# Kernel tuning notes

Hardware: AMD Instinct MI355X
Metric: run time of the kernel (lower is better)

Reference implementation:

```python
import jax, jax.numpy as jnp
import numpy as np

B, L, E, H = 2, 2048, 1024, 16
D = E // H  # head_dim = 64


def setup_inputs() -> dict:
    key = jax.random.key(0)
    ks = jax.random.split(key, 9)
    s = 1.0 / np.sqrt(E)
    return {
        "query": jax.random.normal(ks[0], (B, L, E), jnp.float32),
        "key": jax.random.normal(ks[1], (B, L, E), jnp.float32),
        "value": jax.random.normal(ks[2], (B, L, E), jnp.float32),
        # torch Linear weights are [out_features, in_features]
        "Wq": jax.random.uniform(ks[3], (E, E), jnp.float32, -s, s),
        "bq": jnp.zeros((E,), jnp.float32),
        "Wk": jax.random.uniform(ks[4], (E, E), jnp.float32, -s, s),  # k_proj, no bias (add_bias_kv=False)
        "Wv": jax.random.uniform(ks[5], (E, E), jnp.float32, -s, s),  # v_proj, no bias
        "Wo": jax.random.uniform(ks[6], (E, E), jnp.float32, -s, s),
        "bo": jnp.zeros((E,), jnp.float32),
    }


def reference(query, key, value, Wq, bq, Wk, Wv, Wo, bo):
    # Projections (torch Linear: y = x @ W.T + b)
    q = query @ Wq.T + bq          # [B, L, E]
    k = key @ Wk.T                 # [B, L, E]
    v = value @ Wv.T               # [B, L, E]
    # Split heads
    q = q.reshape(B, L, H, D)
    k = k.reshape(B, L, H, D)
    v = v.reshape(B, L, H, D)
    # Scaled dot-product attention; the source's chunked online-softmax
    # computes exactly softmax(q k^T / sqrt(D)) v.
    q = q / jnp.sqrt(jnp.asarray(D, q.dtype))
    scores = jnp.einsum("bqhd,bkhd->bhqk", q, k)      # [B, H, L, L]
    probs = jax.nn.softmax(scores, axis=-1)
    out = jnp.einsum("bhqk,bkhd->bqhd", probs, v)     # [B, L, H, D]
    out = out.reshape(B, L, E)
    return out @ Wo.T + bo
```

## Files before the change

### kernel.cpp

```cpp
#include <hip/hip_runtime.h>

typedef __bf16 bf16;
typedef __bf16 bf16x8 __attribute__((ext_vector_type(8)));
typedef __bf16 bf16x4 __attribute__((ext_vector_type(4)));
typedef float  f32x4  __attribute__((ext_vector_type(4)));

#define MFMA_BF16(a, b, c) __builtin_amdgcn_mfma_f32_16x16x32_bf16((a), (b), (c), 0, 0, 0)


__device__ __forceinline__ void async_load16(const bf16* g, const bf16* l) {
    auto gp = (const __attribute__((address_space(1))) unsigned int*)(unsigned long long)(const void*)g;
    auto lp = (__attribute__((address_space(3))) unsigned int*)(unsigned int)(unsigned long long)(const void*)l;
    __builtin_amdgcn_global_load_lds(gp, lp, 16, 0, 0);
}

__global__ void cvt_bf16_kernel(
    const float* __restrict__ s0, const float* __restrict__ s1, const float* __restrict__ s2,
    const float* __restrict__ s3, const float* __restrict__ s4, const float* __restrict__ s5,
    const float* __restrict__ s6,
    bf16* __restrict__ d0, bf16* __restrict__ d1, bf16* __restrict__ d2,
    bf16* __restrict__ d3, bf16* __restrict__ d4, bf16* __restrict__ d5,
    bf16* __restrict__ d6)
{
    unsigned e = (blockIdx.x * 256 + threadIdx.x) * 4;
    const float* src; bf16* dst; unsigned off;
    if (e < 12582912u) {
        unsigned which = e >> 22;
        src = which == 0 ? s0 : (which == 1 ? s1 : s2);
        dst = which == 0 ? d0 : (which == 1 ? d1 : d2);
        off = e & 4194303u;
    } else {
        unsigned ew = e - 12582912u;
        unsigned which = ew >> 20;
        src = which == 0 ? s3 : (which == 1 ? s4 : (which == 2 ? s5 : s6));
        dst = which == 0 ? d3 : (which == 1 ? d4 : (which == 2 ? d5 : d6));
        off = ew & 1048575u;
    }
    float4 f = *(const float4*)(src + off);
    bf16x4 o;
    o.x = (bf16)f.x; o.y = (bf16)f.y; o.z = (bf16)f.z; o.w = (bf16)f.w;
    *(bf16x4*)(dst + off) = o;
}

template<int BN>
__global__ __launch_bounds__(256, (BN == 128) ? 2 : 4) void gemm4_kernel(
    const bf16* __restrict__ Xq, const bf16* __restrict__ Xk, const bf16* __restrict__ Xv,
    const bf16* __restrict__ Ao,
    const bf16* __restrict__ Wq, const bf16* __restrict__ Wk, const bf16* __restrict__ Wv,
    const bf16* __restrict__ Wo,
    const float* __restrict__ bq, const float* __restrict__ bo,
    bf16* __restrict__ Qs, bf16* __restrict__ Ksw, bf16* __restrict__ Vsw,
    float* __restrict__ out, int zbase)
{
    const int z = zbase + blockIdx.z;
    const bf16 *Amat, *Bmat;
    if (z == 0)      { Amat = Wq; Bmat = Xq; }
    else if (z == 1) { Amat = Wk; Bmat = Xk; }
    else if (z == 2) { Amat = Xv; Bmat = Wv; }
    else             { Amat = Wo; Bmat = Ao; }

    const int flat = blockIdx.x + 8 * blockIdx.y;
    const int c    = flat & 7;
    const int j    = flat >> 3;
    const int ft   = j & 7;
    const int tt   = c * (gridDim.y >> 3) + (j >> 3);

    const int m0 = (z == 2 ? tt : ft) * 128;
    const int n0 = (z == 2 ? ft : tt) * BN;

    __shared__ __align__(16) bf16 lA[2][128 * 32];
    __shared__ __align__(16) bf16 lB[2][BN * 32];

    const int tid  = threadIdx.x;
    const int w    = tid >> 6;
    const int lane = tid & 63;
    const int lm   = lane & 15;
    const int g    = lane >> 4;
    const int wm   = (w & 1) * 64;
    const int wn   = (w >> 1) * (BN / 2);
    constexpr int NT = BN / 32;
    constexpr int T  = (128 + BN) / 64;

    f32x4 acc[4][NT] = {};

    for (int kb2 = 0; kb2 < 16; kb2++) {
        __syncthreads();
#pragma unroll
        for (int st = 0; st < 2; st++) {
            int kb = kb2 * 2 + st;
#pragma unroll
            for (int t = 0; t < T; t++) {
                int s   = (t * 4 + w) * 64 + lane;
                int row = s >> 2;
                int gs  = s & 3;
                int gg  = gs ^ ((row >> 1) & 3);
                if (row < 128)
                    async_load16(Amat + (size_t)(m0 + row) * 1024 + kb * 32 + gg * 8,
                                 lA[st] + s * 8);
                else
                    async_load16(Bmat + (size_t)(n0 + row - 128) * 1024 + kb * 32 + gg * 8,
                                 lB[st] + (s - 512) * 8);
            }
        }
        __syncthreads();

#pragma unroll
        for (int st = 0; st < 2; st++) {
            bf16x8 af[4], bfr[NT];
#pragma unroll
            for (int mt = 0; mt < 4; mt++) {
                int row = wm + mt * 16 + lm;
                af[mt] = *(const bf16x8*)(lA[st] + row * 32 + ((g ^ ((row >> 1) & 3)) << 3));
            }
#pragma unroll
            for (int nt = 0; nt < NT; nt++) {
                int row = wn + nt * 16 + lm;
                bfr[nt] = *(const bf16x8*)(lB[st] + row * 32 + ((g ^ ((row >> 1) & 3)) << 3));
            }
#pragma unroll
            for (int mt = 0; mt < 4; mt++)
#pragma unroll
                for (int nt = 0; nt < NT; nt++)
                    acc[mt][nt] = MFMA_BF16(af[mt], bfr[nt], acc[mt][nt]);
        }
    }

    if (z == 3) {
#pragma unroll
        for (int mt = 0; mt < 4; mt++) {
            int mb = m0 + wm + mt * 16 + g * 4;
            f32x4 bov = *(const f32x4*)(bo + mb);
#pragma unroll
            for (int nt = 0; nt < NT; nt++) {
                int n = n0 + wn + nt * 16 + lm;
                f32x4 val;
#pragma unroll
                for (int r = 0; r < 4; r++) val[r] = acc[mt][nt][r] + bov[r];
                *(f32x4*)(out + (size_t)n * 1024 + mb) = val;
            }
        }
    } else if (z == 2) {
#pragma unroll
        for (int mt = 0; mt < 4; mt++) {
            int mb   = m0 + wm + mt * 16 + g * 4;
            int b    = mb >> 11;
            int lpos = mb & 2047;
            int kb2  = lpos >> 6, kc = (lpos >> 5) & 1, gv = (lpos >> 3) & 3, j0 = lpos & 7;
#pragma unroll
            for (int nt = 0; nt < NT; nt++) {
                int n = n0 + wn + nt * 16 + lm;
                int h = n >> 6, mt2 = (n >> 4) & 3, lmv = n & 15;
                bf16x4 ov;
#pragma unroll
                for (int r = 0; r < 4; r++) ov[r] = (bf16)acc[mt][nt][r];
                *(bf16x4*)(Vsw + (size_t)(b * 16 + h) * 131072 +
                           (size_t)((kb2 * 8 + mt2 * 2 + kc) * 64 + gv * 16 + lmv) * 8 + j0) = ov;
            }
        }
    } else if (z == 1) {
#pragma unroll
        for (int mt = 0; mt < 4; mt++) {
            int mb = m0 + wm + mt * 16 + g * 4;
            int h  = mb >> 6;
            int f  = (mb >> 5) & 1, gk = (mb >> 3) & 3, j0 = mb & 7;
#pragma unroll
            for (int nt = 0; nt < NT; nt++) {
                int n    = n0 + wn + nt * 16 + lm;
                int b    = n >> 11;
                int lpos = n & 2047;
                int kb2  = lpos >> 6;
                int rem  = lpos & 63;
                int cc   = ((rem >> 4) & 2) | ((rem >> 2) & 1);
                int lmk  = ((rem >> 1) & 12) | (rem & 3);
                bf16x4 ov;
#pragma unroll
                for (int r = 0; r < 4; r++) ov[r] = (bf16)acc[mt][nt][r];
                *(bf16x4*)(Ksw + (size_t)(b * 16 + h) * 131072 +
                           (size_t)((kb2 * 8 + cc * 2 + f) * 64 + gk * 16 + lmk) * 8 + j0) = ov;
            }
        }
    } else {
        const float qscale = 0.18033688011112042f;
#pragma unroll
        for (int mt = 0; mt < 4; mt++) {
            int mb  = m0 + wm + mt * 16 + g * 4;
            int h   = mb >> 6;
            int dd0 = mb & 63;
            f32x4 bqv = *(const f32x4*)(bq + mb);
#pragma unroll
            for (int nt = 0; nt < NT; nt++) {
                int n    = n0 + wn + nt * 16 + lm;
                int b    = n >> 11;
                int lpos = n & 2047;
                bf16x4 ov;
#pragma unroll
                for (int r = 0; r < 4; r++)
                    ov[r] = (bf16)((acc[mt][nt][r] + bqv[r]) * qscale);
                *(bf16x4*)(Qs + (size_t)((b * 16 + h) * 2048 + lpos) * 64 + dd0) = ov;
            }
        }
    }
}

__global__ __launch_bounds__(512, 2) void attn_kernel(
    const bf16* __restrict__ Qs, const bf16* __restrict__ Ksw,
    const bf16* __restrict__ Vsw, bf16* __restrict__ attn)
{
    const int tid  = threadIdx.x;
    const int w    = tid >> 6;
    const int wq   = w & 3;
    const int wk   = w >> 2;
    const int lane = tid & 63;
    const int lm   = lane & 15;
    const int g    = lane >> 4;
    const int i    = blockIdx.x;
    const int bh   = ((i & 7) << 2) | ((i >> 3) & 3);
    const int q0   = (i >> 5) * 256 + wq * 64;

    const bf16* Qh = Qs  + (size_t)bh * 131072;
    const bf16* Kh = Ksw + (size_t)bh * 131072 + (size_t)wk * 65536;
    const bf16* Vh = Vsw + (size_t)bh * 131072 + (size_t)wk * 65536;

    __shared__ __align__(16) float psum[4][64][68];
    __shared__ __align__(16) bf16 ost[4][64 * 72];

    bf16x8 qf[4][2];
#pragma unroll
    for (int qi = 0; qi < 4; qi++)
#pragma unroll
        for (int f = 0; f < 2; f++)
            qf[qi][f] = *(const bf16x8*)(Qh + (size_t)(q0 + qi * 16 + lm) * 64 + f * 32 + g * 8);

    const f32x4 fzero = {0.0f, 0.0f, 0.0f, 0.0f};
    f32x4 o[4][4] = {};
    f32x4 ol[4] = {};
    const bf16x8 ones = {(bf16)1.0f, (bf16)1.0f, (bf16)1.0f, (bf16)1.0f,
                         (bf16)1.0f, (bf16)1.0f, (bf16)1.0f, (bf16)1.0f};

    bf16x8 kf[8], vf[8];
#pragma unroll
    for (int t = 0; t < 8; t++)
        kf[t] = *(const bf16x8*)(Kh + ((size_t)t * 64 + lane) * 8);
#pragma unroll
    for (int t = 0; t < 8; t++)
        vf[t] = *(const bf16x8*)(Vh + ((size_t)t * 64 + lane) * 8);

    for (int kb = 0; kb < 16; kb++) {
        const int kn = (kb < 15) ? kb + 1 : 15;
        const bf16* Kn = Kh + (size_t)kn * 4096;
        const bf16* Vn = Vh + (size_t)kn * 4096;

        bf16x8 pb[4][2];
#pragma unroll
        for (int qi = 0; qi < 4; qi++) {
            f32x4 s[4];
#pragma unroll
            for (int c = 0; c < 4; c++) {
                s[c] = MFMA_BF16(kf[2 * c],     qf[qi][0], fzero);
                s[c] = MFMA_BF16(kf[2 * c + 1], qf[qi][1], s[c]);
            }
            float p[16];
#pragma unroll
            for (int c = 0; c < 4; c++)
#pragma unroll
                for (int r = 0; r < 4; r++)
                    p[(c >> 1) * 8 + (c & 1) * 4 + r] = __builtin_amdgcn_exp2f(s[c][r]);
#pragma unroll
            for (int kc = 0; kc < 2; kc++)
#pragma unroll
                for (int jj = 0; jj < 8; jj++)
                    pb[qi][kc][jj] = (bf16)p[kc * 8 + jj];
        }

#pragma unroll
        for (int t = 0; t < 8; t++)
            kf[t] = *(const bf16x8*)(Kn + ((size_t)t * 64 + lane) * 8);

#pragma unroll
        for (int kc = 0; kc < 2; kc++) {
#pragma unroll
            for (int mt = 0; mt < 4; mt++) {
                bf16x8 vfv = vf[mt * 2 + kc];
#pragma unroll
                for (int qi = 0; qi < 4; qi++)
                    o[qi][mt] = MFMA_BF16(vfv, pb[qi][kc], o[qi][mt]);
            }
#pragma unroll
            for (int qi = 0; qi < 4; qi++)
                ol[qi] = MFMA_BF16(ones, pb[qi][kc], ol[qi]);
        }

#pragma unroll
        for (int t = 0; t < 8; t++)
            vf[t] = *(const bf16x8*)(Vn + ((size_t)t * 64 + lane) * 8);
    }


    if (w >= 4) {
#pragma unroll
        for (int qi = 0; qi < 4; qi++) {
#pragma unroll
            for (int mt = 0; mt < 4; mt++)
                *(f32x4*)(&psum[wq][qi * 16 + lm][mt * 16 + g * 4]) = o[qi][mt];
            if (g == 0)
                psum[wq][qi * 16 + lm][64] = ol[qi][0];
        }
    }
    __syncthreads();
    if (w < 4) {
        const int b = bh >> 4, h = bh & 15;
        bf16* ostw = ost[wq];
#pragma unroll
        for (int qi = 0; qi < 4; qi++) {
            float tot = ol[qi][0] + psum[wq][qi * 16 + lm][64];
            float inv = 1.0f / tot;
#pragma unroll
            for (int mt = 0; mt < 4; mt++) {
                f32x4 ps = *(const f32x4*)(&psum[wq][qi * 16 + lm][mt * 16 + g * 4]);
                bf16x4 ov;
#pragma unroll
                for (int r = 0; r < 4; r++)
                    ov[r] = (bf16)((o[qi][mt][r] + ps[r]) * inv);
                *(bf16x4*)(ostw + (qi * 16 + lm) * 72 + mt * 16 + g * 4) = ov;
            }
        }
        __builtin_amdgcn_s_waitcnt(0);
#pragma unroll
        for (int it = 0; it < 8; it++) {
            int cc = it * 64 + lane;
            int q  = cc >> 3, ch = cc & 7;
            bf16x8 t = *(const bf16x8*)(ostw + q * 72 + ch * 8);
            *(bf16x8*)(attn + (size_t)(b * 2048 + q0 + q) * 1024 + h * 64 + ch * 8) = t;
        }
    }
}

extern "C" void kernel_launch(void* const* d_in, const int* in_sizes, int n_in,
                              void* d_out, int out_size, void* d_ws, size_t ws_size,
                              hipStream_t stream) {
    const float* query = (const float*)d_in[0];
    const float* key   = (const float*)d_in[1];
    const float* value = (const float*)d_in[2];
    const float* Wq    = (const float*)d_in[3];
    const float* bq    = (const float*)d_in[4];
    const float* Wk    = (const float*)d_in[5];
    const float* Wv    = (const float*)d_in[6];
    const float* Wo    = (const float*)d_in[7];
    const float* bo    = (const float*)d_in[8];

    char* ws = (char*)d_ws;
    bf16* Xq  = (bf16*)(ws);
    bf16* Xk  = (bf16*)(ws + ((size_t)8  << 20));
    bf16* Xv  = (bf16*)(ws + ((size_t)16 << 20));
    bf16* Wqb = (bf16*)(ws + ((size_t)24 << 20));
    bf16* Wkb = (bf16*)(ws + ((size_t)26 << 20));
    bf16* Wvb = (bf16*)(ws + ((size_t)28 << 20));
    bf16* Wob = (bf16*)(ws + ((size_t)30 << 20));
    bf16* Qs  = (bf16*)(ws + ((size_t)32 << 20));
    bf16* Ksw = (bf16*)(ws + ((size_t)40 << 20));
    bf16* Vsw = (bf16*)(ws + ((size_t)48 << 20));
    bf16* attn = Xq;

    cvt_bf16_kernel<<<dim3(16384, 1, 1), 256, 0, stream>>>(
        query, key, value, Wq, Wk, Wv, Wo, Xq, Xk, Xv, Wqb, Wkb, Wvb, Wob);

    gemm4_kernel<128><<<dim3(8, 32, 3), 256, 0, stream>>>(
        Xq, Xk, Xv, attn, Wqb, Wkb, Wvb, Wob, bq, bo, Qs, Ksw, Vsw, (float*)d_out, 0);

    attn_kernel<<<dim3(256, 1, 1), 512, 0, stream>>>(Qs, Ksw, Vsw, attn);

    gemm4_kernel<64><<<dim3(8, 64, 1), 256, 0, stream>>>(
        Xq, Xk, Xv, attn, Wqb, Wkb, Wvb, Wob, bq, bo, Qs, Ksw, Vsw, (float*)d_out, 3);
}
```

Baseline: 199.1 us.

## Software-pipeline attention loop: overlap PV MFMAs of block k with QK/exp of k+1

Restructures the per-wave key-block loop into a two-stage software pipeline with double-buffered probability registers (pbA/pbB). The PV MFMAs for the current block are interleaved per output tile with the QK MFMAs and exp2 of the next block, and V/K loads are issued piecewise between them. The goal is to hide exp/convert latency and global load latency behind MFMA work. The cost is more live registers, which could reduce occupancy or cause spills.

```diff
diff --git a/kernel.cpp b/kernel.cpp
--- a/kernel.cpp
+++ b/kernel.cpp
@@ -238,62 +238,86 @@
                          (bf16)1.0f, (bf16)1.0f, (bf16)1.0f, (bf16)1.0f};
 
     bf16x8 kf[8], vf[8];
-#pragma unroll
-    for (int t = 0; t < 8; t++)
-        kf[t] = *(const bf16x8*)(Kh + ((size_t)t * 64 + lane) * 8);
+    bf16x8 pbA[4][2], pbB[4][2];
+
+#define QKSM(qi, PB) do {                                                       \
+    f32x4 s0 = MFMA_BF16(kf[0], qf[qi][0], fzero); s0 = MFMA_BF16(kf[1], qf[qi][1], s0); \
+    f32x4 s1 = MFMA_BF16(kf[2], qf[qi][0], fzero); s1 = MFMA_BF16(kf[3], qf[qi][1], s1); \
+    f32x4 s2 = MFMA_BF16(kf[4], qf[qi][0], fzero); s2 = MFMA_BF16(kf[5], qf[qi][1], s2); \
+    f32x4 s3 = MFMA_BF16(kf[6], qf[qi][0], fzero); s3 = MFMA_BF16(kf[7], qf[qi][1], s3); \
+    _Pragma("unroll")                                                           \
+    for (int r = 0; r < 4; r++) PB[qi][0][r]     = (bf16)__builtin_amdgcn_exp2f(s0[r]); \
+    _Pragma("unroll")                                                           \
+    for (int r = 0; r < 4; r++) PB[qi][0][r + 4] = (bf16)__builtin_amdgcn_exp2f(s1[r]); \
+    _Pragma("unroll")                                                           \
+    for (int r = 0; r < 4; r++) PB[qi][1][r]     = (bf16)__builtin_amdgcn_exp2f(s2[r]); \
+    _Pragma("unroll")                                                           \
+    for (int r = 0; r < 4; r++) PB[qi][1][r + 4] = (bf16)__builtin_amdgcn_exp2f(s3[r]); \
+} while (0)
+
+#define PV_MT(mt, PB) do {                                                      \
+    _Pragma("unroll")                                                           \
+    for (int kc = 0; kc < 2; kc++) {                                            \
+        bf16x8 vfv = vf[(mt) * 2 + kc];                                         \
+        _Pragma("unroll")                                                       \
+        for (int qi = 0; qi < 4; qi++)                                          \
+            o[qi][mt] = MFMA_BF16(vfv, PB[qi][kc], o[qi][mt]);                  \
+    }                                                                           \
+} while (0)
+
+#define PV_ONES(PB) do {                                                        \
+    _Pragma("unroll")                                                           \
+    for (int kc = 0; kc < 2; kc++)                                              \
+        _Pragma("unroll")                                                       \
+        for (int qi = 0; qi < 4; qi++)                                          \
+            ol[qi] = MFMA_BF16(ones, PB[qi][kc], ol[qi]);                       \
+} while (0)
+
+#define VLOAD2(mt, Vn) do {                                                     \
+    vf[(mt) * 2]     = *(const bf16x8*)((Vn) + ((size_t)((mt) * 2)     * 64 + lane) * 8); \
+    vf[(mt) * 2 + 1] = *(const bf16x8*)((Vn) + ((size_t)((mt) * 2 + 1) * 64 + lane) * 8); \
+} while (0)
+
+#define KLOAD(Kn) do {                                                          \
+    _Pragma("unroll")                                                           \
+    for (int t = 0; t < 8; t++)                                                 \
+        kf[t] = *(const bf16x8*)((Kn) + ((size_t)t * 64 + lane) * 8);           \
+} while (0)
+
+#define ITER(kb, PBC, PBN) do {                                                 \
+    const bf16* Vn_ = Vh + (size_t)((kb) + 1) * 4096;                           \
+    const int   kn_ = ((kb) + 2 < 15) ? (kb) + 2 : 15;                          \
+    const bf16* Kn_ = Kh + (size_t)kn_ * 4096;                                  \
+    PV_MT(0, PBC); VLOAD2(0, Vn_); QKSM(0, PBN);                                \
+    PV_MT(1, PBC); VLOAD2(1, Vn_); QKSM(1, PBN);                                \
+    PV_MT(2, PBC); VLOAD2(2, Vn_); QKSM(2, PBN);                                \
+    PV_MT(3, PBC); VLOAD2(3, Vn_); QKSM(3, PBN);                                \
+    PV_ONES(PBC);                                                               \
+    KLOAD(Kn_);                                                                 \
+} while (0)
+
+    KLOAD(Kh);
 #pragma unroll
     for (int t = 0; t < 8; t++)
         vf[t] = *(const bf16x8*)(Vh + ((size_t)t * 64 + lane) * 8);
-
-    for (int kb = 0; kb < 16; kb++) {
-        const int kn = (kb < 15) ? kb + 1 : 15;
-        const bf16* Kn = Kh + (size_t)kn * 4096;
-        const bf16* Vn = Vh + (size_t)kn * 4096;
-
-        bf16x8 pb[4][2];
-#pragma unroll
-        for (int qi = 0; qi < 4; qi++) {
-            f32x4 s[4];
-#pragma unroll
-            for (int c = 0; c < 4; c++) {
-                s[c] = MFMA_BF16(kf[2 * c],     qf[qi][0], fzero);
-                s[c] = MFMA_BF16(kf[2 * c + 1], qf[qi][1], s[c]);
-            }
-            float p[16];
-#pragma unroll
-            for (int c = 0; c < 4; c++)
-#pragma unroll
-                for (int r = 0; r < 4; r++)
-                    p[(c >> 1) * 8 + (c & 1) * 4 + r] = __builtin_amdgcn_exp2f(s[c][r]);
-#pragma unroll
-            for (int kc = 0; kc < 2; kc++)
-#pragma unroll
-                for (int jj = 0; jj < 8; jj++)
-                    pb[qi][kc][jj] = (bf16)p[kc * 8 + jj];
-        }
-
-#pragma unroll
-        for (int t = 0; t < 8; t++)
-            kf[t] = *(const bf16x8*)(Kn + ((size_t)t * 64 + lane) * 8);
-
-#pragma unroll
-        for (int kc = 0; kc < 2; kc++) {
-#pragma unroll
-            for (int mt = 0; mt < 4; mt++) {
-                bf16x8 vfv = vf[mt * 2 + kc];
-#pragma unroll
-                for (int qi = 0; qi < 4; qi++)
-                    o[qi][mt] = MFMA_BF16(vfv, pb[qi][kc], o[qi][mt]);
-            }
-#pragma unroll
-            for (int qi = 0; qi < 4; qi++)
-                ol[qi] = MFMA_BF16(ones, pb[qi][kc], ol[qi]);
-        }
-
-#pragma unroll
-        for (int t = 0; t < 8; t++)
-            vf[t] = *(const bf16x8*)(Vn + ((size_t)t * 64 + lane) * 8);
-    }
+    QKSM(0, pbA); QKSM(1, pbA); QKSM(2, pbA); QKSM(3, pbA);
+    KLOAD(Kh + 4096);
+
+    for (int kb2 = 0; kb2 < 7; kb2++) {
+        ITER(2 * kb2,     pbA, pbB);
+        ITER(2 * kb2 + 1, pbB, pbA);
+    }
+    ITER(14, pbA, pbB);
+
+    PV_MT(0, pbB); PV_MT(1, pbB); PV_MT(2, pbB); PV_MT(3, pbB);
+    PV_ONES(pbB);
+
+#undef ITER
+#undef KLOAD
+#undef VLOAD2
+#undef PV_ONES
+#undef PV_MT
+#undef QKSM
 
 
     if (w >= 4) {
```

New measurement: 234.2 us. 1.18x slower.
